# Optimization experiments

Hardware: AMD Instinct MI355X
Metric: run time of the kernel (lower is better)

The kernel has to match this reference:

```python
import jax, jax.numpy as jnp
import numpy as np

B, L, D, H, R = 2, 128, 256, 8, 4
DK = D // H  # 32
EPS = 1e-6


def setup_inputs() -> dict:
    key = jax.random.key(0)
    ks = jax.random.split(key, 12)
    q = jax.random.normal(ks[0], (B, L, D), jnp.float32)
    k = jax.random.normal(ks[1], (B, L, D), jnp.float32)
    v = jax.random.normal(ks[2], (B, L, D), jnp.float32)
    t = jnp.sort(jax.random.uniform(ks[3], (B, L), jnp.float32), axis=-1)
    omega = jax.random.uniform(ks[4], (B, L, L), jnp.float32)
    mask = jnp.triu(jnp.ones((L, L), bool), 1)  # True = masked (causal)
    xav = (2.0 / (D + D)) ** 0.5
    Wq = jax.random.normal(ks[5], (D, H * DK), jnp.float32) * xav
    Wk = jax.random.normal(ks[6], (D, H * DK), jnp.float32) * xav
    Wv = jax.random.normal(ks[7], (D, H * DK), jnp.float32) * xav
    s = jax.random.uniform(ks[8], (R,), jnp.float32) + 0.1  # ODE time-decay scales
    fc_w = jax.random.normal(ks[9], (H * DK, D), jnp.float32) * xav
    fc_b = jnp.zeros((D,), jnp.float32)
    ln_g = jnp.ones((D,), jnp.float32)
    ln_b = jnp.zeros((D,), jnp.float32)
    return {"q": q, "k": k, "v": v, "t": t, "omega": omega, "mask": mask,
            "Wq": Wq, "Wk": Wk, "Wv": Wv, "s": s,
            "fc_w": fc_w, "fc_b": fc_b, "ln_g": ln_g, "ln_b": ln_b}


def _ode_proj(x, W, phi):
    # x: (B,L,D), W: (D,H*DK), phi: (B,L,L,R) time kernel
    p = x @ W                                       # (B,L,H*DK)
    y = p[:, None, :, None, :] * phi[..., None]     # (B,L,L,R,H*DK)
    y = y.reshape(B, L, L, R, H, DK)
    return y.transpose(0, 4, 1, 2, 3, 5)            # (B,H,L,L,R,DK)


def reference(q, k, v, t, omega, mask, Wq, Wk, Wv, s, fc_w, fc_b, ln_g, ln_b):
    temp = DK ** 0.5
    residual = q
    # pre-LayerNorm on q (normalize_before=True)
    mu = q.mean(-1, keepdims=True)
    var = q.var(-1, keepdims=True)
    qn = (q - mu) / jnp.sqrt(var + EPS) * ln_g + ln_b
    # continuous-time kernel phi[b,i,j,r] = exp(-|t_i - t_j| * s_r)
    dt = jnp.abs(t[:, :, None] - t[:, None, :])     # (B,L,L)
    phi = jnp.exp(-dt[..., None] * s)               # (B,L,L,R)
    q6 = _ode_proj(qn, Wq, phi)                     # (B,H,L,L,R,DK)
    k6 = _ode_proj(k, Wk, phi)
    v6 = _ode_proj(v, Wv, phi)
    # attn = (q/temp * k * omega).sum(-1).sum(-1)
    attn = jnp.einsum('bhijrd,bhijrd,bij->bhij', q6 / temp, k6, omega)
    attn = jnp.where(mask[None, None, :, :], -1e9, attn)
    attn = jax.nn.softmax(attn, axis=-1)            # (B,H,L,L)
    vsum = v6.sum(axis=4)                           # sum over R -> (B,H,L,L,DK)
    out = jnp.einsum('bhij,bhijd->bhid', attn, vsum)  # (B,H,L,DK)
    out = out.transpose(0, 2, 1, 3).reshape(B, L, H * DK)
    out = out @ fc_w + fc_b + residual              # dropout = identity (eval)
    return (out, attn)
```

## Files before the change

kernel.cpp:

```cpp
#include <hip/hip_runtime.h>

#define B_  2
#define L_  128
#define D_  256
#define H_  8
#define R_  4
#define BL_ (B_*L_)
#define SXP 260


__device__ __forceinline__ float wredsum64(float v) {
    #pragma unroll
    for (int m = 32; m >= 1; m >>= 1) v += __shfl_xor(v, m, 64);
    return v;
}
__device__ __forceinline__ float wredmax64(float v) {
    #pragma unroll
    for (int m = 32; m >= 1; m >>= 1) v = fmaxf(v, __shfl_xor(v, m, 64));
    return v;
}

__global__ __launch_bounds__(256) void k_proj(
    const float* __restrict__ q, const float* __restrict__ k, const float* __restrict__ v,
    const float* __restrict__ Wq, const float* __restrict__ Wk, const float* __restrict__ Wv,
    const float* __restrict__ ln_g, const float* __restrict__ ln_b,
    float* __restrict__ pv, float* __restrict__ qkpart)
{
    const int blk = blockIdx.x;
    const int rowTile = blk >> 4;
    const int cg = blk & 15;
    const int rbase = rowTile * 4;
    const int tid = threadIdx.x;

    __shared__ __align__(16) float sx[3][4 * SXP];
    __shared__ __align__(16) float partF[16 * 4 * 16];
    __shared__ float spq[4][16], spk[4][16];

    {
        const int r = tid >> 6, f4c = tid & 63;
        #pragma unroll
        for (int p = 0; p < 3; ++p) {
            const float* src = (p == 0 ? q : (p == 1 ? k : v)) + (size_t)(rbase + r) * D_;
            *reinterpret_cast<float4*>(&sx[p][r * SXP + f4c * 4]) =
                reinterpret_cast<const float4*>(src)[f4c];
        }
    }
    __syncthreads();

    {
        const int r = tid >> 6, lane = tid & 63;
        float x0 = sx[0][r * SXP + lane];
        float x1 = sx[0][r * SXP + lane + 64];
        float x2 = sx[0][r * SXP + lane + 128];
        float x3 = sx[0][r * SXP + lane + 192];
        float s1 = x0 + x1 + x2 + x3;
        float s2 = x0*x0 + x1*x1 + x2*x2 + x3*x3;
        #pragma unroll
        for (int m = 32; m >= 1; m >>= 1) {
            s1 += __shfl_xor(s1, m, 64);
            s2 += __shfl_xor(s2, m, 64);
        }
        const float mu = s1 * (1.0f / D_);
        const float rs = rsqrtf(s2 * (1.0f / D_) - mu * mu + 1e-6f);
        sx[0][r * SXP + lane      ] = (x0 - mu) * rs * ln_g[lane      ] + ln_b[lane      ];
        sx[0][r * SXP + lane +  64] = (x1 - mu) * rs * ln_g[lane +  64] + ln_b[lane +  64];
        sx[0][r * SXP + lane + 128] = (x2 - mu) * rs * ln_g[lane + 128] + ln_b[lane + 128];
        sx[0][r * SXP + lane + 192] = (x3 - mu) * rs * ln_g[lane + 192] + ln_b[lane + 192];
    }
    __syncthreads();

    const int kg  = tid >> 4;
    const int row = (tid >> 2) & 3;
    const int c4  = tid & 3;
    const int gc4 = cg * 4 + c4;
    const int kbase = kg * 16;

    #pragma unroll
    for (int m = 0; m < 3; ++m) {
        const float4* W4 = reinterpret_cast<const float4*>(m == 0 ? Wq : (m == 1 ? Wk : Wv));
        float4 a = {0, 0, 0, 0};
        #pragma unroll
        for (int kk = 0; kk < 16; ++kk) {
            const int kr = kbase + kk;
            const float x = sx[m][row * SXP + kr];
            const float4 w = W4[kr * 64 + gc4];
            a.x += x * w.x; a.y += x * w.y; a.z += x * w.z; a.w += x * w.w;
        }
        *reinterpret_cast<float4*>(&partF[(kg * 16 + row * 4 + c4) * 4]) = a;
        __syncthreads();
        if (tid < 64) {
            const int rr = tid >> 4, cc = tid & 15;
            float sum = 0.f;
            #pragma unroll
            for (int g = 0; g < 16; ++g) sum += partF[g * 64 + rr * 16 + cc];
            if      (m == 0) spq[rr][cc] = sum;
            else if (m == 1) spk[rr][cc] = sum;
            else             pv[(size_t)(rbase + rr) * D_ + cg * 16 + cc] = sum;
        }
        __syncthreads();
    }

    if (tid < 64) {
        const int rr = tid >> 4, cc = tid & 15;
        float d = spq[rr][cc] * spk[rr][cc];
        #pragma unroll
        for (int m = 8; m >= 1; m >>= 1) d += __shfl_xor(d, m, 64);
        if (cc == 0) qkpart[(size_t)(rbase + rr) * 16 + cg] = d;
    }
}

__global__ __launch_bounds__(256) void k_attn_fc(
    const float* __restrict__ q, const float* __restrict__ t, const float* __restrict__ omega,
    const float* __restrict__ s, const float* __restrict__ fc_w, const float* __restrict__ fc_b,
    const float* __restrict__ pv, const float* __restrict__ qkpart,
    float* __restrict__ dout)
{
    const int blk = blockIdx.x;
    const int b = blk >> 7;
    const int i = blk & (L_ - 1);
    const int tid = threadIdx.x;

    __shared__ __align__(16) float sQKp[L_ * 16];
    __shared__ __align__(16) float sQK[L_ * H_];
    __shared__ __align__(16) float sOm[L_];
    __shared__ __align__(16) float sAttn[H_][L_];
    __shared__ __align__(16) float sMid[D_];
    __shared__ float sPhi[L_], sPsi[L_], st[L_], sS[R_];

    {
        const float4* qkp4 = reinterpret_cast<const float4*>(qkpart + (size_t)b * L_ * 16);
        reinterpret_cast<float4*>(sQKp)[tid]       = qkp4[tid];
        reinterpret_cast<float4*>(sQKp)[tid + 256] = qkp4[tid + 256];
        if (tid < 32) {
            reinterpret_cast<float4*>(sOm)[tid] =
                reinterpret_cast<const float4*>(omega + ((size_t)(b * L_ + i)) * L_)[tid];
            reinterpret_cast<float4*>(st)[tid] =
                reinterpret_cast<const float4*>(t + (size_t)b * L_)[tid];
        }
        if (tid < R_) sS[tid] = s[tid];
    }
    __syncthreads();

    if (tid < 128) {
        #pragma unroll
        for (int h = 0; h < H_; ++h)
            sQK[tid * H_ + h] = sQKp[tid * 16 + 2 * h] + sQKp[tid * 16 + 2 * h + 1];
        const float dtv = fabsf(st[i] - st[tid]);
        float Phi = 0.f, Psi = 0.f;
        #pragma unroll
        for (int r = 0; r < R_; ++r) {
            const float e = expf(-dtv * sS[r]);
            Phi += e;
            Psi += e * e;
        }
        sPhi[tid] = Phi;
        sPsi[tid] = Psi;
    }
    __syncthreads();

    const int w = tid >> 6, lane = tid & 63;
    const float invtemp = 0.17677669529663687f;
    #pragma unroll
    for (int pass = 0; pass < 2; ++pass) {
        const int h = w * 2 + pass;
        const int j0 = lane, j1 = lane + 64;
        float l0 = (j0 <= i) ? sOm[j0] * sPsi[j0] * sQK[j0 * H_ + h] * invtemp : -3.0e38f;
        float l1 = (j1 <= i) ? sOm[j1] * sPsi[j1] * sQK[j1 * H_ + h] * invtemp : -3.0e38f;
        const float mx = wredmax64(fmaxf(l0, l1));
        const float e0 = (j0 <= i) ? expf(l0 - mx) : 0.f;
        const float e1 = (j1 <= i) ? expf(l1 - mx) : 0.f;
        const float inv = 1.0f / wredsum64(e0 + e1);
        const float a0 = e0 * inv, a1 = e1 * inv;
        sAttn[h][j0] = a0;
        sAttn[h][j1] = a1;
        const size_t ab = (size_t)BL_ * D_ + (((size_t)(b * H_ + h) * L_ + i) * L_);
        dout[ab + j0] = a0;
        dout[ab + j1] = a1;
    }
    __syncthreads();

    {
        const int h = tid >> 5;
        const float* pvb = pv + (size_t)b * L_ * D_ + tid;
        float acc = 0.f;
        #pragma unroll 4
        for (int j = 0; j <= i; ++j)
            acc += sAttn[h][j] * sPhi[j] * pvb[j * D_];
        sMid[tid] = acc;
    }
    __syncthreads();

    {
        const size_t orow = (size_t)(b * L_ + i) * D_;
        float r = fc_b[tid] + q[orow + tid];
        const float* fwc = fc_w + tid;
        #pragma unroll 8
        for (int kk = 0; kk < D_; ++kk)
            r += sMid[kk] * fwc[kk * D_];
        dout[orow + tid] = r;
    }
}

extern "C" void kernel_launch(void* const* d_in, const int* in_sizes, int n_in,
                              void* d_out, int out_size, void* d_ws, size_t ws_size,
                              hipStream_t stream) {
    const float* q     = (const float*)d_in[0];
    const float* k     = (const float*)d_in[1];
    const float* v     = (const float*)d_in[2];
    const float* t     = (const float*)d_in[3];
    const float* omega = (const float*)d_in[4];
    const float* Wq    = (const float*)d_in[6];
    const float* Wk    = (const float*)d_in[7];
    const float* Wv    = (const float*)d_in[8];
    const float* s     = (const float*)d_in[9];
    const float* fc_w  = (const float*)d_in[10];
    const float* fc_b  = (const float*)d_in[11];
    const float* ln_g  = (const float*)d_in[12];
    const float* ln_b  = (const float*)d_in[13];

    float* ws     = (float*)d_ws;
    float* pv     = ws;
    float* qkpart = ws + 65536;
    float* out    = (float*)d_out;

    hipLaunchKernelGGL(k_proj, dim3(1024), dim3(256), 0, stream,
                       q, k, v, Wq, Wk, Wv, ln_g, ln_b, pv, qkpart);
    hipLaunchKernelGGL(k_attn_fc, dim3(256), dim3(256), 0, stream,
                       q, t, omega, s, fc_w, fc_b, pv, qkpart, out);
}
```

Measured before the change: 103.5 us.

## Split attention-FC blocks by column half and parallelize PV/FC reductions over j/k

k_attn_fc now launches two blocks per query row, each recomputing the softmax but writing only half the attention heads and half the output columns. The serial j-loop for attn·PV and the serial k-loop for the FC are replaced by split-k float4 partial sums staged in shared memory and reduced afterward. k_proj stores all three projection partials first and reduces them with a single barrier pair instead of one per matrix. The aim is to cut the long dependent loop latency and raise occupancy. The cost is redundant softmax and PV work per half block, plus extra shared memory.

Result: slower. 109.0 us (+5.4%).

```diff
diff --git a/kernel.cpp b/kernel.cpp
--- a/kernel.cpp
+++ b/kernel.cpp
@@ -33,7 +33,7 @@
     const int tid = threadIdx.x;
 
     __shared__ __align__(16) float sx[3][4 * SXP];
-    __shared__ __align__(16) float partF[16 * 4 * 16];
+    __shared__ __align__(16) float partF[3][16 * 64];
     __shared__ float spq[4][16], spk[4][16];
 
     {
@@ -86,19 +86,21 @@
             const float4 w = W4[kr * 64 + gc4];
             a.x += x * w.x; a.y += x * w.y; a.z += x * w.z; a.w += x * w.w;
         }
-        *reinterpret_cast<float4*>(&partF[(kg * 16 + row * 4 + c4) * 4]) = a;
-        __syncthreads();
-        if (tid < 64) {
-            const int rr = tid >> 4, cc = tid & 15;
-            float sum = 0.f;
-            #pragma unroll
-            for (int g = 0; g < 16; ++g) sum += partF[g * 64 + rr * 16 + cc];
-            if      (m == 0) spq[rr][cc] = sum;
-            else if (m == 1) spk[rr][cc] = sum;
-            else             pv[(size_t)(rbase + rr) * D_ + cg * 16 + cc] = sum;
-        }
-        __syncthreads();
-    }
+        *reinterpret_cast<float4*>(&partF[m][(kg * 16 + row * 4 + c4) * 4]) = a;
+    }
+    __syncthreads();
+
+    if (tid < 192) {
+        const int m = tid >> 6, c = tid & 63;
+        const int rr = c >> 4, cc = c & 15;
+        float sum = 0.f;
+        #pragma unroll
+        for (int g = 0; g < 16; ++g) sum += partF[m][g * 64 + c];
+        if      (m == 0) spq[rr][cc] = sum;
+        else if (m == 1) spk[rr][cc] = sum;
+        else             pv[(size_t)(rbase + rr) * D_ + cg * 16 + cc] = sum;
+    }
+    __syncthreads();
 
     if (tid < 64) {
         const int rr = tid >> 4, cc = tid & 15;
@@ -116,8 +118,9 @@
     float* __restrict__ dout)
 {
     const int blk = blockIdx.x;
-    const int b = blk >> 7;
-    const int i = blk & (L_ - 1);
+    const int b    = blk >> 8;
+    const int i    = (blk >> 1) & (L_ - 1);
+    const int half = blk & 1;
     const int tid = threadIdx.x;
 
     __shared__ __align__(16) float sQKp[L_ * 16];
@@ -125,6 +128,7 @@
     __shared__ __align__(16) float sOm[L_];
     __shared__ __align__(16) float sAttn[H_][L_];
     __shared__ __align__(16) float sMid[D_];
+    __shared__ __align__(16) float partB[16 * 256];
     __shared__ float sPhi[L_], sPsi[L_], st[L_], sS[R_];
 
     {
@@ -173,31 +177,75 @@
         const float a0 = e0 * inv, a1 = e1 * inv;
         sAttn[h][j0] = a0;
         sAttn[h][j1] = a1;
-        const size_t ab = (size_t)BL_ * D_ + (((size_t)(b * H_ + h) * L_ + i) * L_);
-        dout[ab + j0] = a0;
-        dout[ab + j1] = a1;
-    }
-    __syncthreads();
-
-    {
-        const int h = tid >> 5;
-        const float* pvb = pv + (size_t)b * L_ * D_ + tid;
-        float acc = 0.f;
-        #pragma unroll 4
-        for (int j = 0; j <= i; ++j)
-            acc += sAttn[h][j] * sPhi[j] * pvb[j * D_];
-        sMid[tid] = acc;
-    }
-    __syncthreads();
-
-    {
+        if ((h >> 2) == half) {
+            const size_t ab = (size_t)BL_ * D_ + (((size_t)(b * H_ + h) * L_ + i) * L_);
+            dout[ab + j0] = a0;
+            dout[ab + j1] = a1;
+        }
+    }
+    __syncthreads();
+
+    {
+        const int jg = tid >> 4, cq = tid & 15;
+        const int h2 = cq >> 1;
+        const float4* pv4 = reinterpret_cast<const float4*>(pv + (size_t)b * L_ * D_);
+        float4 acc[4];
+        #pragma unroll
+        for (int c = 0; c < 4; ++c) acc[c] = make_float4(0, 0, 0, 0);
+        #pragma unroll
+        for (int kjj = 0; kjj < 8; ++kjj) {
+            const int j = jg + kjj * 16;
+            const float wgt = sAttn[h2][j] * sPhi[j];
+            #pragma unroll
+            for (int c = 0; c < 4; ++c) {
+                const float4 p = pv4[j * 64 + cq * 4 + c];
+                acc[c].x += wgt * p.x; acc[c].y += wgt * p.y;
+                acc[c].z += wgt * p.z; acc[c].w += wgt * p.w;
+            }
+        }
+        #pragma unroll
+        for (int c = 0; c < 4; ++c)
+            *reinterpret_cast<float4*>(&partB[jg * 256 + cq * 16 + c * 4]) = acc[c];
+    }
+    __syncthreads();
+    {
+        float sum = 0.f;
+        #pragma unroll
+        for (int g = 0; g < 16; ++g) sum += partB[g * 256 + tid];
+        sMid[tid] = sum;
+    }
+    __syncthreads();
+
+    {
+        const int kg = tid >> 3, cq = tid & 7;
+        const float4* fw4 = reinterpret_cast<const float4*>(fc_w);
+        float4 acc[4];
+        #pragma unroll
+        for (int c = 0; c < 4; ++c) acc[c] = make_float4(0, 0, 0, 0);
+        #pragma unroll
+        for (int kk = 0; kk < 8; ++kk) {
+            const int kr = kg + kk * 32;
+            const float x = sMid[kr];
+            #pragma unroll
+            for (int c = 0; c < 4; ++c) {
+                const float4 wv = fw4[kr * 64 + half * 32 + cq * 4 + c];
+                acc[c].x += x * wv.x; acc[c].y += x * wv.y;
+                acc[c].z += x * wv.z; acc[c].w += x * wv.w;
+            }
+        }
+        #pragma unroll
+        for (int c = 0; c < 4; ++c)
+            *reinterpret_cast<float4*>(&partB[kg * 128 + cq * 16 + c * 4]) = acc[c];
+    }
+    __syncthreads();
+
+    if (tid < 128) {
+        const int col = half * 128 + tid;
         const size_t orow = (size_t)(b * L_ + i) * D_;
-        float r = fc_b[tid] + q[orow + tid];
-        const float* fwc = fc_w + tid;
-        #pragma unroll 8
-        for (int kk = 0; kk < D_; ++kk)
-            r += sMid[kk] * fwc[kk * D_];
-        dout[orow + tid] = r;
+        float sum = fc_b[col] + q[orow + col];
+        #pragma unroll
+        for (int g = 0; g < 32; ++g) sum += partB[g * 128 + tid];
+        dout[orow + col] = sum;
     }
 }
 
@@ -225,6 +273,6 @@
 
     hipLaunchKernelGGL(k_proj, dim3(1024), dim3(256), 0, stream,
                        q, k, v, Wq, Wk, Wv, ln_g, ln_b, pv, qkpart);
-    hipLaunchKernelGGL(k_attn_fc, dim3(256), dim3(256), 0, stream,
+    hipLaunchKernelGGL(k_attn_fc, dim3(512), dim3(256), 0, stream,
                        q, t, omega, s, fc_w, fc_b, pv, qkpart, out);
 }
```
